# Optimization experiments

Hardware: AMD Instinct MI355X
Metric: run time of the kernel (lower is better)

The kernel has to match this reference:

```python
import jax, jax.numpy as jnp
import numpy as np

CLASS_COST = 2.0
BBOX_COST = 5.0
GIOU_COST = 2.0
ALPHA = 0.25
GAMMA = 2.0
EPS = 1e-08


def center_to_corners(b):
    # b: [..., 4] in (cx, cy, w, h) -> (x0, y0, x1, y1)
    cx, cy, w, h = b[..., 0], b[..., 1], b[..., 2], b[..., 3]
    return jnp.stack([cx - 0.5 * w, cy - 0.5 * h, cx + 0.5 * w, cy + 0.5 * h], axis=-1)


def generalized_box_iou(boxes1, boxes2):
    # boxes1: [N,4], boxes2: [M,4], corners format -> [N,M] GIoU
    area1 = (boxes1[:, 2] - boxes1[:, 0]) * (boxes1[:, 3] - boxes1[:, 1])
    area2 = (boxes2[:, 2] - boxes2[:, 0]) * (boxes2[:, 3] - boxes2[:, 1])
    lt = jnp.maximum(boxes1[:, None, :2], boxes2[None, :, :2])  # [N,M,2]
    rb = jnp.minimum(boxes1[:, None, 2:], boxes2[None, :, 2:])
    wh = jnp.clip(rb - lt, 0.0)
    inter = wh[..., 0] * wh[..., 1]  # [N,M]
    union = area1[:, None] + area2[None, :] - inter
    iou = inter / union
    lt_e = jnp.minimum(boxes1[:, None, :2], boxes2[None, :, :2])
    rb_e = jnp.maximum(boxes1[:, None, 2:], boxes2[None, :, 2:])
    wh_e = jnp.clip(rb_e - lt_e, 0.0)
    area_e = wh_e[..., 0] * wh_e[..., 1]
    return iou - (area_e - union) / area_e


def setup_inputs() -> dict:
    key = jax.random.key(0)
    k1, k2, k3, k4, k5 = jax.random.split(key, 5)
    B, Q, C, T, L = 16, 900, 512, 40, 91
    return {
        "logits": jax.random.normal(k1, (B, Q, C), dtype=jnp.float32),
        "pred_boxes": jax.random.uniform(k2, (B, Q, 4), dtype=jnp.float32),
        "label_maps": jax.random.uniform(k3, (B, L, C), dtype=jnp.float32),
        "boxes": jax.random.uniform(k4, (B, T, 4), dtype=jnp.float32),
        "class_labels": jax.random.randint(k5, (B, T), 0, L, dtype=jnp.int32),
    }


def reference(logits, pred_boxes, label_maps, boxes, class_labels):
    B, Q, C = logits.shape
    T = boxes.shape[1]
    out_prob = jax.nn.sigmoid(logits.reshape(B * Q, C))          # [BQ, C]
    out_bbox = pred_boxes.reshape(B * Q, 4)
    # gather per-batch label maps, then normalize
    lm = jax.vmap(lambda m, idx: m[idx])(label_maps, class_labels)  # [B, T, C]
    lm = lm.reshape(B * T, C)
    lm = lm / lm.sum(axis=-1, keepdims=True)
    target_bbox = boxes.reshape(B * T, 4)
    # focal-style class cost
    neg_cost = (1 - ALPHA) * out_prob ** GAMMA * (-jnp.log(1 - out_prob + EPS))
    pos_cost = ALPHA * (1 - out_prob) ** GAMMA * (-jnp.log(out_prob + EPS))
    class_cost = (pos_cost - neg_cost) @ lm.T                    # [BQ, BT]
    bbox_cost = jnp.sum(jnp.abs(out_bbox[:, None, :] - target_bbox[None, :, :]), axis=-1)
    giou_cost = -generalized_box_iou(center_to_corners(out_bbox), center_to_corners(target_bbox))
    cost = BBOX_COST * bbox_cost + CLASS_COST * class_cost + GIOU_COST * giou_cost
    return cost.reshape(B, Q, B * T)
```

## Files before the change

### kernel.cpp

```cpp
#include <hip/hip_runtime.h>
#include <hip/hip_bf16.h>

#define BQ   14400
#define BT   640
#define CD   512
#define LD   91
#define TD   40

typedef __attribute__((ext_vector_type(8))) short short8;
typedef __attribute__((ext_vector_type(4))) float f32x4;

__global__ __launch_bounds__(256) void build_lm_kernel(
    const float* __restrict__ label_maps,
    const int* __restrict__ class_labels,
    __hip_bfloat16* __restrict__ lm)
{
    int j = blockIdx.x;
    int b = j / TD;
    int cls = class_labels[j];
    const float* src = label_maps + ((size_t)b * LD + cls) * CD;
    int t = threadIdx.x;
    float v0 = src[t];
    float v1 = src[t + 256];
    float s = v0 + v1;
    #pragma unroll
    for (int off = 32; off >= 1; off >>= 1) s += __shfl_down(s, off, 64);
    __shared__ float red[4];
    if ((t & 63) == 0) red[t >> 6] = s;
    __syncthreads();
    float inv = 1.0f / (red[0] + red[1] + red[2] + red[3]);
    lm[(size_t)j * CD + t]       = __float2bfloat16(v0 * inv);
    lm[(size_t)j * CD + t + 256] = __float2bfloat16(v1 * inv);
}

__global__ __launch_bounds__(256) void build_focal_kernel(
    const float* __restrict__ logits,
    __hip_bfloat16* __restrict__ F)
{
    size_t i = ((size_t)blockIdx.x * 256 + threadIdx.x) * 4;
    float4 x = *(const float4*)(logits + i);
    float xs[4] = {x.x, x.y, x.z, x.w};
    union { __hip_bfloat16 h[4]; uint2 u; } pk;
    #pragma unroll
    for (int k = 0; k < 4; ++k) {
        float p = 1.0f / (1.0f + __expf(-xs[k]));
        float pos = 0.25f * (1.0f - p) * (1.0f - p) * (-__logf(p + 1e-8f));
        float neg = 0.75f * p * p * (-__logf(1.0f - p + 1e-8f));
        pk.h[k] = __float2bfloat16(pos - neg);
    }
    *(uint2*)(F + i) = pk.u;
}

__global__ __launch_bounds__(256) void cost_gemm_kernel(
    const __hip_bfloat16* __restrict__ F,
    const __hip_bfloat16* __restrict__ lm,
    const float* __restrict__ pred_boxes,
    const float* __restrict__ tboxes,
    float* __restrict__ out)
{
    __shared__ short As[64][40];
    __shared__ short Bs[64][40];
    __shared__ float pB[64][4];
    __shared__ float tB[64][4];

    int m0 = blockIdx.x * 64;
    int n0 = blockIdx.y * 64;
    int t  = threadIdx.x;

    {
        int r = t >> 2, c = t & 3;
        pB[r][c] = pred_boxes[(size_t)(m0 + r) * 4 + c];
        tB[r][c] = tboxes[(size_t)(n0 + r) * 4 + c];
    }

    int lane = t & 63;
    int w    = t >> 6;
    int wr   = w >> 1, wc = w & 1;
    int lrow = lane & 15;
    int kg   = lane >> 4;

    f32x4 acc[2][2] = {};

    int sr = t >> 2;
    int sk = (t & 3) * 8;
    const __hip_bfloat16* gA = F  + (size_t)(m0 + sr) * CD + sk;
    const __hip_bfloat16* gB = lm + (size_t)(n0 + sr) * CD + sk;

    for (int kk = 0; kk < CD; kk += 32) {
        uint4 av = *(const uint4*)(gA + kk);
        uint4 bv = *(const uint4*)(gB + kk);
        __syncthreads();
        *(uint4*)(&As[sr][sk]) = av;
        *(uint4*)(&Bs[sr][sk]) = bv;
        __syncthreads();
        short8 a0 = *(const short8*)(&As[wr * 32      + lrow][kg * 8]);
        short8 a1 = *(const short8*)(&As[wr * 32 + 16 + lrow][kg * 8]);
        short8 b0 = *(const short8*)(&Bs[wc * 32      + lrow][kg * 8]);
        short8 b1 = *(const short8*)(&Bs[wc * 32 + 16 + lrow][kg * 8]);
        acc[0][0] = __builtin_amdgcn_mfma_f32_16x16x32_bf16(a0, b0, acc[0][0], 0, 0, 0);
        acc[0][1] = __builtin_amdgcn_mfma_f32_16x16x32_bf16(a0, b1, acc[0][1], 0, 0, 0);
        acc[1][0] = __builtin_amdgcn_mfma_f32_16x16x32_bf16(a1, b0, acc[1][0], 0, 0, 0);
        acc[1][1] = __builtin_amdgcn_mfma_f32_16x16x32_bf16(a1, b1, acc[1][1], 0, 0, 0);
    }

    #pragma unroll
    for (int ni = 0; ni < 2; ++ni) {
        int cl = wc * 32 + ni * 16 + lrow;
        float tcx = tB[cl][0], tcy = tB[cl][1], tw = tB[cl][2], th = tB[cl][3];
        float tx0 = tcx - 0.5f * tw, ty0 = tcy - 0.5f * th;
        float tx1 = tcx + 0.5f * tw, ty1 = tcy + 0.5f * th;
        float areaT = (tx1 - tx0) * (ty1 - ty0);
        #pragma unroll
        for (int mi = 0; mi < 2; ++mi) {
            #pragma unroll
            for (int r = 0; r < 4; ++r) {
                int rl = wr * 32 + mi * 16 + kg * 4 + r;
                float pcx = pB[rl][0], pcy = pB[rl][1], pw = pB[rl][2], ph = pB[rl][3];
                float px0 = pcx - 0.5f * pw, py0 = pcy - 0.5f * ph;
                float px1 = pcx + 0.5f * pw, py1 = pcy + 0.5f * ph;
                float areaP = (px1 - px0) * (py1 - py0);
                float bbox = fabsf(pcx - tcx) + fabsf(pcy - tcy)
                           + fabsf(pw - tw)  + fabsf(ph - th);
                float ltx = fmaxf(px0, tx0), lty = fmaxf(py0, ty0);
                float rbx = fminf(px1, tx1), rby = fminf(py1, ty1);
                float iw = fmaxf(rbx - ltx, 0.0f), ih = fmaxf(rby - lty, 0.0f);
                float inter = iw * ih;
                float uni = areaP + areaT - inter;
                float iou = inter / uni;
                float ex0 = fminf(px0, tx0), ey0 = fminf(py0, ty0);
                float ex1 = fmaxf(px1, tx1), ey1 = fmaxf(py1, ty1);
                float areaE = fmaxf(ex1 - ex0, 0.0f) * fmaxf(ey1 - ey0, 0.0f);
                float giou = iou - (areaE - uni) / areaE;
                float cls = acc[mi][ni][r];
                out[(size_t)(m0 + rl) * BT + (n0 + cl)] =
                    5.0f * bbox + 2.0f * cls + 2.0f * (-giou);
            }
        }
    }
}

extern "C" void kernel_launch(void* const* d_in, const int* in_sizes, int n_in,
                              void* d_out, int out_size, void* d_ws, size_t ws_size,
                              hipStream_t stream) {
    const float* logits      = (const float*)d_in[0];
    const float* pred_boxes  = (const float*)d_in[1];
    const float* label_maps  = (const float*)d_in[2];
    const float* boxes       = (const float*)d_in[3];
    const int*   class_labels= (const int*)d_in[4];
    float* out = (float*)d_out;

    __hip_bfloat16* F  = (__hip_bfloat16*)d_ws;
    __hip_bfloat16* lm = (__hip_bfloat16*)((char*)d_ws
                          + (size_t)BQ * CD * sizeof(__hip_bfloat16));

    build_lm_kernel<<<BT, 256, 0, stream>>>(label_maps, class_labels, lm);
    build_focal_kernel<<<(BQ * CD / 4) / 256, 256, 0, stream>>>(logits, F);
    dim3 grid(BQ / 64, BT / 64);
    cost_gemm_kernel<<<grid, 256, 0, stream>>>(F, lm, pred_boxes, boxes, out);
}
```

Before: 134.4 us.

## Fuse focal-term computation into cost GEMM with pre-fragmented label-map operand

Merges the focal preprocessing into the GEMM kernel, so each block computes its 64 rows of focal terms straight into LDS with an XOR swizzle and never writes the bf16 intermediate to global memory. The label-map kernel now emits B already laid out in MFMA fragment order, so each wave reads its B fragments directly from global memory. Each block covers all 640 columns with 8 waves of 2x10 MFMA tiles, and the box epilogue precomputes per-row terms and replaces divides with fast reciprocals. This removes the F round-trip and the per-k-step LDS staging and barriers, at the cost of heavy register use, fast-math approximations and a clamped logit range in the focal term.

```diff
diff --git a/kernel.cpp b/kernel.cpp
--- a/kernel.cpp
+++ b/kernel.cpp
@@ -10,130 +10,181 @@
 typedef __attribute__((ext_vector_type(8))) short short8;
 typedef __attribute__((ext_vector_type(4))) float f32x4;
 
-__global__ __launch_bounds__(256) void build_lm_kernel(
+__global__ __launch_bounds__(256) void build_lmfrag_kernel(
     const float* __restrict__ label_maps,
     const int* __restrict__ class_labels,
-    __hip_bfloat16* __restrict__ lm)
+    __hip_bfloat16* __restrict__ Bf)
 {
-    int j = blockIdx.x;
-    int b = j / TD;
-    int cls = class_labels[j];
-    const float* src = label_maps + ((size_t)b * LD + cls) * CD;
-    int t = threadIdx.x;
-    float v0 = src[t];
-    float v1 = src[t + 256];
-    float s = v0 + v1;
-    #pragma unroll
-    for (int off = 32; off >= 1; off >>= 1) s += __shfl_down(s, off, 64);
-    __shared__ float red[4];
-    if ((t & 63) == 0) red[t >> 6] = s;
+    __shared__ float rows[16][512];
+    __shared__ float inv[16];
+    int nt = blockIdx.x;
+    int t  = threadIdx.x;
+
+    #pragma unroll
+    for (int e = 0; e < 8; ++e) {
+        int idx4 = t + e * 256;
+        int r    = idx4 >> 7;
+        int c4   = idx4 & 127;
+        int j    = nt * 16 + r;
+        int b    = j / TD;
+        int cls  = class_labels[j];
+        float4 v = *(const float4*)(label_maps + ((size_t)(b * LD + cls) * CD) + c4 * 4);
+        *(float4*)(&rows[r][c4 * 4]) = v;
+    }
     __syncthreads();
-    float inv = 1.0f / (red[0] + red[1] + red[2] + red[3]);
-    lm[(size_t)j * CD + t]       = __float2bfloat16(v0 * inv);
-    lm[(size_t)j * CD + t + 256] = __float2bfloat16(v1 * inv);
-}
-
-__global__ __launch_bounds__(256) void build_focal_kernel(
+
+    int w = t >> 6, l = t & 63;
+    #pragma unroll
+    for (int q = 0; q < 4; ++q) {
+        int r = w * 4 + q;
+        float s = 0.f;
+        #pragma unroll
+        for (int e = 0; e < 8; ++e) s += rows[r][l + e * 64];
+        #pragma unroll
+        for (int off = 32; off >= 1; off >>= 1) s += __shfl_down(s, off, 64);
+        if (l == 0) inv[r] = __builtin_amdgcn_rcpf(s);
+    }
+    __syncthreads();
+
+    #pragma unroll
+    for (int e = 0; e < 4; ++e) {
+        int sc = t + e * 256;
+        int kb = sc >> 6;
+        int ln = sc & 63;
+        int o  = ln >> 4;
+        int rr = ln & 15;
+        float scale = inv[rr];
+        union { __hip_bfloat16 h[8]; uint4 u; } pk;
+        #pragma unroll
+        for (int j2 = 0; j2 < 8; ++j2)
+            pk.h[j2] = __float2bfloat16(rows[rr][kb * 32 + o * 8 + j2] * scale);
+        *(uint4*)((char*)Bf + ((size_t)nt * 1024 + sc) * 16) = pk.u;
+    }
+}
+
+__device__ __forceinline__ float focal_term(float x)
+{
+    x = fminf(fmaxf(x, -18.0f), 18.0f);
+    float q   = __expf(-x);
+    float s   = 1.0f + q;
+    float p   = __builtin_amdgcn_rcpf(s);
+    float spn = __logf(s);
+    float omp = q * p;
+    float pos = 0.25f * omp * omp * spn;
+    float neg = 0.75f * p * p * (x + spn);
+    return pos - neg;
+}
+
+__global__ __launch_bounds__(512, 2) void fused_cost_kernel(
     const float* __restrict__ logits,
-    __hip_bfloat16* __restrict__ F)
-{
-    size_t i = ((size_t)blockIdx.x * 256 + threadIdx.x) * 4;
-    float4 x = *(const float4*)(logits + i);
-    float xs[4] = {x.x, x.y, x.z, x.w};
-    union { __hip_bfloat16 h[4]; uint2 u; } pk;
-    #pragma unroll
-    for (int k = 0; k < 4; ++k) {
-        float p = 1.0f / (1.0f + __expf(-xs[k]));
-        float pos = 0.25f * (1.0f - p) * (1.0f - p) * (-__logf(p + 1e-8f));
-        float neg = 0.75f * p * p * (-__logf(1.0f - p + 1e-8f));
-        pk.h[k] = __float2bfloat16(pos - neg);
-    }
-    *(uint2*)(F + i) = pk.u;
-}
-
-__global__ __launch_bounds__(256) void cost_gemm_kernel(
-    const __hip_bfloat16* __restrict__ F,
-    const __hip_bfloat16* __restrict__ lm,
     const float* __restrict__ pred_boxes,
+    const __hip_bfloat16* __restrict__ Bf,
     const float* __restrict__ tboxes,
     float* __restrict__ out)
 {
-    __shared__ short As[64][40];
-    __shared__ short Bs[64][40];
+    __shared__ __align__(16) short A[64][512];
     __shared__ float pB[64][4];
-    __shared__ float tB[64][4];
-
+    __shared__ float tB[BT][4];
+
+    int t  = threadIdx.x;
     int m0 = blockIdx.x * 64;
-    int n0 = blockIdx.y * 64;
-    int t  = threadIdx.x;
+
+    if (t < 64)  *(float4*)(&pB[t][0]) = *(const float4*)(pred_boxes + (size_t)(m0 + t) * 4);
+    *(float4*)(&tB[t][0]) = *(const float4*)(tboxes + (size_t)t * 4);
+    if (t < BT - 512) *(float4*)(&tB[512 + t][0]) = *(const float4*)(tboxes + (size_t)(512 + t) * 4);
 
     {
-        int r = t >> 2, c = t & 3;
-        pB[r][c] = pred_boxes[(size_t)(m0 + r) * 4 + c];
-        tB[r][c] = tboxes[(size_t)(n0 + r) * 4 + c];
-    }
-
-    int lane = t & 63;
+        int row = t >> 3;
+        int sl  = t & 7;
+        int r7  = row & 7;
+        const float* lp = logits + (size_t)(m0 + row) * CD + sl * 16;
+        #pragma unroll
+        for (int i = 0; i < 4; ++i) {
+            union { float4 v4[4]; float f[16]; } xu;
+            #pragma unroll
+            for (int j = 0; j < 4; ++j) xu.v4[j] = *(const float4*)(lp + i * 128 + j * 4);
+            union { __hip_bfloat16 h[16]; uint4 u[2]; } pk;
+            #pragma unroll
+            for (int k = 0; k < 16; ++k) pk.h[k] = __float2bfloat16(focal_term(xu.f[k]));
+            int o0 = sl * 2 + i * 16;
+            *(uint4*)(&A[row][(o0 ^ r7) * 8])       = pk.u[0];
+            *(uint4*)(&A[row][((o0 + 1) ^ r7) * 8]) = pk.u[1];
+        }
+    }
+    __syncthreads();
+
+    int l    = t & 63;
     int w    = t >> 6;
-    int wr   = w >> 1, wc = w & 1;
-    int lrow = lane & 15;
-    int kg   = lane >> 4;
-
-    f32x4 acc[2][2] = {};
-
-    int sr = t >> 2;
-    int sk = (t & 3) * 8;
-    const __hip_bfloat16* gA = F  + (size_t)(m0 + sr) * CD + sk;
-    const __hip_bfloat16* gB = lm + (size_t)(n0 + sr) * CD + sk;
-
-    for (int kk = 0; kk < CD; kk += 32) {
-        uint4 av = *(const uint4*)(gA + kk);
-        uint4 bv = *(const uint4*)(gB + kk);
-        __syncthreads();
-        *(uint4*)(&As[sr][sk]) = av;
-        *(uint4*)(&Bs[sr][sk]) = bv;
-        __syncthreads();
-        short8 a0 = *(const short8*)(&As[wr * 32      + lrow][kg * 8]);
-        short8 a1 = *(const short8*)(&As[wr * 32 + 16 + lrow][kg * 8]);
-        short8 b0 = *(const short8*)(&Bs[wc * 32      + lrow][kg * 8]);
-        short8 b1 = *(const short8*)(&Bs[wc * 32 + 16 + lrow][kg * 8]);
-        acc[0][0] = __builtin_amdgcn_mfma_f32_16x16x32_bf16(a0, b0, acc[0][0], 0, 0, 0);
-        acc[0][1] = __builtin_amdgcn_mfma_f32_16x16x32_bf16(a0, b1, acc[0][1], 0, 0, 0);
-        acc[1][0] = __builtin_amdgcn_mfma_f32_16x16x32_bf16(a1, b0, acc[1][0], 0, 0, 0);
-        acc[1][1] = __builtin_amdgcn_mfma_f32_16x16x32_bf16(a1, b1, acc[1][1], 0, 0, 0);
-    }
-
-    #pragma unroll
-    for (int ni = 0; ni < 2; ++ni) {
-        int cl = wc * 32 + ni * 16 + lrow;
+    int wr   = w & 1;
+    int wcg  = w >> 1;
+    int lrow = l & 15;
+    int kg   = l >> 4;
+    int r7a  = lrow & 7;
+    int arow0 = wr * 32 + lrow;
+    int arow1 = arow0 + 16;
+
+    f32x4 acc[2][10] = {};
+    const short8* bp = (const short8*)Bf + (size_t)wcg * 10240 + l;
+
+    #pragma unroll 2
+    for (int kb = 0; kb < 16; ++kb) {
+        short8 a0 = *(const short8*)(&A[arow0][((kb * 4 + kg) ^ r7a) * 8]);
+        short8 a1 = *(const short8*)(&A[arow1][((kb * 4 + kg) ^ r7a) * 8]);
+        short8 bfr[10];
+        #pragma unroll
+        for (int nf = 0; nf < 10; ++nf) bfr[nf] = bp[nf * 1024 + kb * 64];
+        #pragma unroll
+        for (int nf = 0; nf < 10; ++nf) {
+            acc[0][nf] = __builtin_amdgcn_mfma_f32_16x16x32_bf16(a0, bfr[nf], acc[0][nf], 0, 0, 0);
+            acc[1][nf] = __builtin_amdgcn_mfma_f32_16x16x32_bf16(a1, bfr[nf], acc[1][nf], 0, 0, 0);
+        }
+    }
+
+    float rp[8][9];
+    #pragma unroll
+    for (int rf = 0; rf < 2; ++rf) {
+        #pragma unroll
+        for (int r = 0; r < 4; ++r) {
+            int rl = wr * 32 + rf * 16 + kg * 4 + r;
+            float pcx = pB[rl][0], pcy = pB[rl][1], pw = pB[rl][2], ph = pB[rl][3];
+            float* P = rp[rf * 4 + r];
+            P[0] = pcx; P[1] = pcy; P[2] = pw; P[3] = ph;
+            P[4] = pcx - 0.5f * pw;
+            P[5] = pcy - 0.5f * ph;
+            P[6] = pcx + 0.5f * pw;
+            P[7] = pcy + 0.5f * ph;
+            P[8] = pw * ph;
+        }
+    }
+
+    #pragma unroll
+    for (int nf = 0; nf < 10; ++nf) {
+        int cl = wcg * 160 + nf * 16 + lrow;
         float tcx = tB[cl][0], tcy = tB[cl][1], tw = tB[cl][2], th = tB[cl][3];
         float tx0 = tcx - 0.5f * tw, ty0 = tcy - 0.5f * th;
         float tx1 = tcx + 0.5f * tw, ty1 = tcy + 0.5f * th;
-        float areaT = (tx1 - tx0) * (ty1 - ty0);
-        #pragma unroll
-        for (int mi = 0; mi < 2; ++mi) {
+        float areaT = tw * th;
+        #pragma unroll
+        for (int rf = 0; rf < 2; ++rf) {
             #pragma unroll
             for (int r = 0; r < 4; ++r) {
-                int rl = wr * 32 + mi * 16 + kg * 4 + r;
-                float pcx = pB[rl][0], pcy = pB[rl][1], pw = pB[rl][2], ph = pB[rl][3];
-                float px0 = pcx - 0.5f * pw, py0 = pcy - 0.5f * ph;
-                float px1 = pcx + 0.5f * pw, py1 = pcy + 0.5f * ph;
-                float areaP = (px1 - px0) * (py1 - py0);
-                float bbox = fabsf(pcx - tcx) + fabsf(pcy - tcy)
-                           + fabsf(pw - tw)  + fabsf(ph - th);
-                float ltx = fmaxf(px0, tx0), lty = fmaxf(py0, ty0);
-                float rbx = fminf(px1, tx1), rby = fminf(py1, ty1);
-                float iw = fmaxf(rbx - ltx, 0.0f), ih = fmaxf(rby - lty, 0.0f);
+                const float* P = rp[rf * 4 + r];
+                float bbox = fabsf(P[0] - tcx) + fabsf(P[1] - tcy)
+                           + fabsf(P[2] - tw)  + fabsf(P[3] - th);
+                float iw = fminf(P[6], tx1) - fmaxf(P[4], tx0);
+                float ih = fminf(P[7], ty1) - fmaxf(P[5], ty0);
+                iw = fmaxf(iw, 0.0f); ih = fmaxf(ih, 0.0f);
                 float inter = iw * ih;
-                float uni = areaP + areaT - inter;
-                float iou = inter / uni;
-                float ex0 = fminf(px0, tx0), ey0 = fminf(py0, ty0);
-                float ex1 = fmaxf(px1, tx1), ey1 = fmaxf(py1, ty1);
-                float areaE = fmaxf(ex1 - ex0, 0.0f) * fmaxf(ey1 - ey0, 0.0f);
-                float giou = iou - (areaE - uni) / areaE;
-                float cls = acc[mi][ni][r];
-                out[(size_t)(m0 + rl) * BT + (n0 + cl)] =
-                    5.0f * bbox + 2.0f * cls + 2.0f * (-giou);
+                float uni   = P[8] + areaT - inter;
+                float ew = fmaxf(P[6], tx1) - fminf(P[4], tx0);
+                float eh = fmaxf(P[7], ty1) - fminf(P[5], ty0);
+                float areaE = ew * eh;
+                float iou  = inter * __builtin_amdgcn_rcpf(uni);
+                float gpen = (areaE - uni) * __builtin_amdgcn_rcpf(areaE);
+                float giou = iou - gpen;
+                float cls  = acc[rf][nf][r];
+                int rl = wr * 32 + rf * 16 + kg * 4 + r;
+                out[(size_t)(m0 + rl) * BT + cl] = 5.0f * bbox + 2.0f * cls - 2.0f * giou;
             }
         }
     }
@@ -142,19 +193,15 @@
 extern "C" void kernel_launch(void* const* d_in, const int* in_sizes, int n_in,
                               void* d_out, int out_size, void* d_ws, size_t ws_size,
                               hipStream_t stream) {
-    const float* logits      = (const float*)d_in[0];
-    const float* pred_boxes  = (const float*)d_in[1];
-    const float* label_maps  = (const float*)d_in[2];
-    const float* boxes       = (const float*)d_in[3];
-    const int*   class_labels= (const int*)d_in[4];
+    const float* logits       = (const float*)d_in[0];
+    const float* pred_boxes   = (const float*)d_in[1];
+    const float* label_maps   = (const float*)d_in[2];
+    const float* boxes        = (const float*)d_in[3];
+    const int*   class_labels = (const int*)d_in[4];
     float* out = (float*)d_out;
 
-    __hip_bfloat16* F  = (__hip_bfloat16*)d_ws;
-    __hip_bfloat16* lm = (__hip_bfloat16*)((char*)d_ws
-                          + (size_t)BQ * CD * sizeof(__hip_bfloat16));
-
-    build_lm_kernel<<<BT, 256, 0, stream>>>(label_maps, class_labels, lm);
-    build_focal_kernel<<<(BQ * CD / 4) / 256, 256, 0, stream>>>(logits, F);
-    dim3 grid(BQ / 64, BT / 64);
-    cost_gemm_kernel<<<grid, 256, 0, stream>>>(F, lm, pred_boxes, boxes, out);
-}
+    __hip_bfloat16* Bf = (__hip_bfloat16*)d_ws;
+
+    build_lmfrag_kernel<<<40, 256, 0, stream>>>(label_maps, class_labels, Bf);
+    fused_cost_kernel<<<BQ / 64, 512, 0, stream>>>(logits, pred_boxes, Bf, boxes, out);
+}
```

Result: faster. 120.4 us (-10.4%).
